# Optimization experiments

Measured on AMD Instinct MI355X. Metric: run time of the kernel, lower is better.

Reference implementation:

```python
import jax, jax.numpy as jnp
import numpy as np

LEVELS = 6
_S = float(1.0 / np.sqrt(2.0))  # forward transform scales kernels by 1/sqrt(2)
# Complex Daubechies 6-tap filters (real, imag), pre-scaled for the forward DWT.
LO_R = [v * _S for v in (-0.0662912607, 0.1104854346, 0.6629126074, 0.6629126074, 0.1104854346, -0.0662912607)]
LO_I = [v * _S for v in (-0.0855816496, -0.0855816496, 0.1711632992, 0.1711632992, -0.0855816496, -0.0855816496)]
HI_R = [v * _S for v in (-0.0662912607, -0.1104854346, 0.6629126074, -0.6629126074, 0.1104854346, 0.0662912607)]
HI_I = [v * _S for v in (0.0855816496, -0.0855816496, -0.1711632992, 0.1711632992, 0.0855816496, -0.0855816496)]


def _corr_down(v, k):
    """Circular-padded 6-tap correlation along last axis, stride-2 decimation.
    v: [..., L] (L even) -> [..., L//2]. Matches torch: circular pad 3 each side,
    valid conv (L+1 outputs), then slice 0:-1:2."""
    L = v.shape[-1]
    vp = jnp.concatenate([v[..., -3:], v, v[..., :3]], axis=-1)  # [..., L+6]
    out = k[0] * vp[..., 0:L - 1:2]
    for t in range(1, 6):
        out = out + k[t] * vp[..., t:t + L - 1:2]
    return out


def _cconv_down(xr, xi, kr, ki):
    """Complex conv + downsample: (xr + i*xi) * (kr + i*ki) along last axis."""
    return (_corr_down(xr, kr) - _corr_down(xi, ki),
            _corr_down(xr, ki) + _corr_down(xi, kr))


def _decompose(xr, xi):
    """One DWT level. xr, xi: [B, C, h, w] -> (zr, zi) same shape."""
    # vertical pass: convolve along h (transpose so h is last)
    xrT = xr.swapaxes(-1, -2)  # [B, C, w, h]
    xiT = xi.swapaxes(-1, -2)
    lr, li = _cconv_down(xrT, xiT, LO_R, LO_I)  # [B, C, w, h//2]
    hr, hi = _cconv_down(xrT, xiT, HI_R, HI_I)
    yr = jnp.concatenate([lr, hr], axis=-1).swapaxes(-1, -2)  # [B, C, h, w]
    yi = jnp.concatenate([li, hi], axis=-1).swapaxes(-1, -2)
    # horizontal pass: convolve along w
    lr, li = _cconv_down(yr, yi, LO_R, LO_I)  # [B, C, h, w//2]
    hr, hi = _cconv_down(yr, yi, HI_R, HI_I)
    zr = jnp.concatenate([lr, hr], axis=-1)
    zi = jnp.concatenate([li, hi], axis=-1)
    return zr, zi


def setup_inputs() -> dict:
    key = jax.random.key(0)
    images = jax.random.uniform(key, (8, 3, 1024, 1024), dtype=jnp.float32)
    return {"images": images}


def reference(images):
    B, C, H, W = images.shape
    xr = images
    xi = jnp.zeros_like(images)
    res_r = jnp.zeros((B, C, H, W), images.dtype)
    res_i = jnp.zeros((B, C, H, W), images.dtype)
    for i in range(LEVELS):
        h, w = H >> i, W >> i
        if i == 0:
            sr, si = xr, xi
        else:
            sr, si = res_r[..., :h, :w], res_i[..., :h, :w]
        dr, di = _decompose(sr, si)
        res_r = res_r.at[..., :h, :w].set(dr)
        res_i = res_i.at[..., :h, :w].set(di)
    return jnp.stack([res_r, res_i], axis=2)  # [B, C, 2, H, W]
```

## Files before the change

kernel.cpp:

```cpp
#include <hip/hip_runtime.h>
#include <type_traits>


#define SQ2 0.7071067811865476

constexpr float kLOR0 = (float)(-0.0662912607 * SQ2);
constexpr float kLOR1 = (float)( 0.1104854346 * SQ2);
constexpr float kLOR2 = (float)( 0.6629126074 * SQ2);
constexpr float kLOI0 = (float)(-0.0855816496 * SQ2);
constexpr float kLOI1 = (float)(-0.0855816496 * SQ2);
constexpr float kLOI2 = (float)( 0.1711632992 * SQ2);
constexpr float kHIR0 = (float)(-0.0662912607 * SQ2);
constexpr float kHIR1 = (float)(-0.1104854346 * SQ2);
constexpr float kHIR2 = (float)( 0.6629126074 * SQ2);
constexpr float kHII0 = (float)( 0.0855816496 * SQ2);
constexpr float kHII1 = (float)(-0.0855816496 * SQ2);
constexpr float kHII2 = (float)(-0.1711632992 * SQ2);

typedef float f4v __attribute__((ext_vector_type(4)));
typedef float f2v __attribute__((ext_vector_type(2)));

template <bool IM>
__device__ __forceinline__ void cconv6(const float* xr, const float* xi,
                                       float& lr, float& li, float& hr,
                                       float& hi) {
  const float s0 = xr[0] + xr[5], s1 = xr[1] + xr[4], s2 = xr[2] + xr[3];
  const float d0 = xr[0] - xr[5], d1 = xr[1] - xr[4], d2 = xr[2] - xr[3];
  lr = kLOR0 * s0 + kLOR1 * s1 + kLOR2 * s2;
  li = kLOI0 * s0 + kLOI1 * s1 + kLOI2 * s2;
  hr = kHIR0 * d0 + kHIR1 * d1 + kHIR2 * d2;
  hi = kHII0 * d0 + kHII1 * d1 + kHII2 * d2;
  if (IM) {
    const float t0 = xi[0] + xi[5], t1 = xi[1] + xi[4], t2 = xi[2] + xi[3];
    const float e0 = xi[0] - xi[5], e1 = xi[1] - xi[4], e2 = xi[2] - xi[3];
    lr -= kLOI0 * t0 + kLOI1 * t1 + kLOI2 * t2;
    li += kLOR0 * t0 + kLOR1 * t1 + kLOR2 * t2;
    hr -= kHII0 * e0 + kHII1 * e1 + kHII2 * e2;
    hi += kHIR0 * e0 + kHIR1 * e1 + kHIR2 * e2;
  }
}

__device__ __forceinline__ void gload16(const f4v* src, f4v* ldsDst) {
  __builtin_amdgcn_global_load_lds(
      (__attribute__((address_space(1))) const void*)src,
      (__attribute__((address_space(3))) void*)ldsDst, 16, 0, 0);
}

template <int TB, bool HAS_IMAG, bool LL_TO_WS>
__global__ __launch_bounds__(256) void dwt_kernel(
    const float* __restrict__ inR, const float* __restrict__ inI,
    float* __restrict__ out, float* __restrict__ llR, float* __restrict__ llI,
    int h, int w, int tilesPerRow, int tilesPerPlane, int cpx8, int HW,
    int W0) {
  constexpr int RROWS = 2 * TB + 4;
  constexpr int F4PR = TB / 2 + 2;
  constexpr int SW = 4 * F4PR;
  constexpr int NF4 = RROWS * F4PR;
  constexpr int NF4P = ((NF4 + 255) / 256) * 256;
  constexpr int C2 = 2 * TB + 4;
  constexpr int NPASS = TB / 16;
  constexpr int QACT = (TB / 2 < 16) ? TB / 2 : 16;

  __shared__ f4v s4R[NF4P];
  __shared__ f4v s4I[HAS_IMAG ? NF4P : 1];
  __shared__ __align__(16) float yLR[16 * C2], yLI[16 * C2];
  __shared__ __align__(16) float yHR[16 * C2], yHI[16 * C2];

  const int tid = threadIdx.x;
  int bid = (int)blockIdx.x;
  bid = (bid & 7) * cpx8 + (bid >> 3);
  const int plane = bid / tilesPerPlane;
  const int trem = bid - plane * tilesPerPlane;
  const int ti = trem / tilesPerRow;
  const int tj = trem - ti * tilesPerRow;

  const int hm = h - 1;
  const int w4 = w >> 2, w4m = w4 - 1;
  const int rowstart = 2 * TB * ti - 3;
  const int col4start = (TB / 2) * tj - 1;

  const float* pinR = inR + (size_t)plane * h * w;
  const float* pinI = HAS_IMAG ? (inI + (size_t)plane * h * w) : nullptr;

  {
    const int lane = tid & 63;
    const int wid = tid >> 6;
    for (int c0 = wid * 64; c0 < NF4P; c0 += 256) {
      const int idx = c0 + lane;
      const int rr = idx / F4PR;
      const int qq = idx - rr * F4PR;
      const int gr = (rowstart + rr) & hm;
      const int gq = (col4start + qq) & w4m;
      const size_t goff = (size_t)gr * w4 + gq;
      gload16((const f4v*)pinR + goff, &s4R[c0]);
      if (HAS_IMAG) gload16((const f4v*)pinI + goff, &s4I[c0]);
    }
  }
  __syncthreads();

  const float* sRf = (const float*)s4R;
  const float* sIf = (const float*)s4I;
  const int i0 = TB * ti, j0g = TB * tj;
  const int h2 = h >> 1, w2 = w >> 1;
  float* outR = out + (size_t)plane * 2 * HW;
  float* outI = outR + HW;

  const int wv = tid >> 6;
  const int lane = tid & 63;
  const int r = lane >> 4, q = lane & 15;

  for (int p = 0; p < NPASS; ++p) {
    const int ibase = p * 16 + wv * 4;

    {
      auto s2col = [&](int c) {
        const float* cR = sRf + (2 * ibase) * SW + c + 1;
        const float* cI = sIf + (2 * ibase) * SW + c + 1;
        float xr[12], xi[12];
#pragma unroll
        for (int m = 0; m < 12; ++m) {
          xr[m] = cR[m * SW];
          if (HAS_IMAG) xi[m] = cI[m * SW];
        }
#pragma unroll
        for (int k = 0; k < 4; ++k) {
          float lr, li, hr, hi;
          cconv6<HAS_IMAG>(&xr[2 * k], &xi[2 * k], lr, li, hr, hi);
          const int yi = (wv * 4 + k) * C2 + c;
          yLR[yi] = lr;
          yLI[yi] = li;
          yHR[yi] = hr;
          yHI[yi] = hi;
        }
      };
      if (C2 >= 64) {
        s2col(lane);
        if (lane < 4 * (C2 - 64)) {
          const int ce = 64 + (lane >> 2);
          const int ke = lane & 3;
          const float* cR = sRf + (2 * (ibase + ke)) * SW + ce + 1;
          const float* cI = sIf + (2 * (ibase + ke)) * SW + ce + 1;
          float xr[6], xi[6];
#pragma unroll
          for (int m = 0; m < 6; ++m) {
            xr[m] = cR[m * SW];
            if (HAS_IMAG) xi[m] = cI[m * SW];
          }
          float lr, li, hr, hi;
          cconv6<HAS_IMAG>(xr, xi, lr, li, hr, hi);
          const int yi = (wv * 4 + ke) * C2 + ce;
          yLR[yi] = lr;
          yLI[yi] = li;
          yHR[yi] = hr;
          yHI[yi] = hi;
        }
      } else {
        if (lane < C2) s2col(lane);
      }
    }
    asm volatile("s_waitcnt lgkmcnt(0)" ::: "memory");
    __builtin_amdgcn_sched_barrier(0);

    if (q < QACT) {
      const int slot = wv * 4 + r;
      const int base = slot * C2 + 4 * q;
      float xLR[8], xLI[8], xHR[8], xHI[8];
      *(f4v*)&xLR[0] = *(const f4v*)&yLR[base];
      *(f4v*)&xLR[4] = *(const f4v*)&yLR[base + 4];
      *(f4v*)&xLI[0] = *(const f4v*)&yLI[base];
      *(f4v*)&xLI[4] = *(const f4v*)&yLI[base + 4];
      *(f4v*)&xHR[0] = *(const f4v*)&yHR[base];
      *(f4v*)&xHR[4] = *(const f4v*)&yHR[base + 4];
      *(f4v*)&xHI[0] = *(const f4v*)&yHI[base];
      *(f4v*)&xHI[4] = *(const f4v*)&yHI[base + 4];
      float o[8][2];
#pragma unroll
      for (int u = 0; u < 2; ++u) {
        cconv6<true>(&xLR[2 * u], &xLI[2 * u], o[0][u], o[1][u], o[2][u],
                     o[3][u]);
        cconv6<true>(&xHR[2 * u], &xHI[2 * u], o[4][u], o[5][u], o[6][u],
                     o[7][u]);
      }
      const int gi = i0 + ibase + r;
      const int gj = j0g + 2 * q;
      const int rlo = gi, rhi = h2 + gi, clo = gj, chi = w2 + gj;
      auto st = [&](float* pdst, int v) {
        f2v t;
        t.x = o[v][0];
        t.y = o[v][1];
        __builtin_nontemporal_store(t, (f2v*)pdst);
      };
      st(outR + (size_t)rlo * W0 + chi, 2);
      st(outI + (size_t)rlo * W0 + chi, 3);
      st(outR + (size_t)rhi * W0 + clo, 4);
      st(outI + (size_t)rhi * W0 + clo, 5);
      st(outR + (size_t)rhi * W0 + chi, 6);
      st(outI + (size_t)rhi * W0 + chi, 7);
      if (LL_TO_WS) {
        const size_t off = (size_t)plane * h2 * w2 + (size_t)gi * w2 + gj;
        f2v a, b;
        a.x = o[0][0];
        a.y = o[0][1];
        b.x = o[1][0];
        b.y = o[1][1];
        *(f2v*)(llR + off) = a;
        *(f2v*)(llI + off) = b;
      } else {
        st(outR + (size_t)rlo * W0 + clo, 0);
        st(outI + (size_t)rlo * W0 + clo, 1);
      }
    }
  }
}

extern "C" void kernel_launch(void* const* d_in, const int* in_sizes, int n_in,
                              void* d_out, int out_size, void* d_ws,
                              size_t ws_size, hipStream_t stream) {
  const float* images = (const float*)d_in[0];
  float* out = (float*)d_out;
  constexpr int B = 8, C = 3, H = 1024, W = 1024;
  constexpr int NP = B * C;

  float* wsf = (float*)d_ws;
  const size_t S0 = (size_t)NP * 512 * 512;
  const size_t S1 = (size_t)NP * 256 * 256;
  float* buf0R = wsf;
  float* buf0I = wsf + S0;
  float* buf1R = wsf + 2 * S0;
  float* buf1I = wsf + 2 * S0 + S1;

  auto launch = [&](auto tb_tag, bool hasImag, bool llToWs, const float* iR,
                    const float* iI, float* lR, float* lI, int hsz) {
    constexpr int TB = decltype(tb_tag)::value;
    const int tpr = (hsz / 2) / TB;
    const int tpp = tpr * tpr;
    const int grid = NP * tpp;
    if (!hasImag) {
      dwt_kernel<TB, false, true><<<grid, 256, 0, stream>>>(
          iR, nullptr, out, lR, lI, hsz, hsz, tpr, tpp, grid / 8, H * W, W);
    } else if (llToWs) {
      dwt_kernel<TB, true, true><<<grid, 256, 0, stream>>>(
          iR, iI, out, lR, lI, hsz, hsz, tpr, tpp, grid / 8, H * W, W);
    } else {
      dwt_kernel<TB, true, false><<<grid, 256, 0, stream>>>(
          iR, iI, out, nullptr, nullptr, hsz, hsz, tpr, tpp, grid / 8, H * W,
          W);
    }
  };

  launch(std::integral_constant<int, 32>{}, false, true, images, nullptr,
         buf0R, buf0I, 1024);
  launch(std::integral_constant<int, 32>{}, true, true, buf0R, buf0I, buf1R,
         buf1I, 512);
  launch(std::integral_constant<int, 32>{}, true, true, buf1R, buf1I, buf0R,
         buf0I, 256);
  launch(std::integral_constant<int, 32>{}, true, true, buf0R, buf0I, buf1R,
         buf1I, 128);
  launch(std::integral_constant<int, 16>{}, true, true, buf1R, buf1I, buf0R,
         buf0I, 64);
  launch(std::integral_constant<int, 16>{}, true, false, buf0R, buf0I,
         nullptr, nullptr, 32);
}
```

Before: 89.02 us.

## Repartition per-wave work to two rows and one output column per lane

```diff
diff --git a/kernel.cpp b/kernel.cpp
--- a/kernel.cpp
+++ b/kernel.cpp
@@ -58,13 +58,12 @@
   constexpr int NF4 = RROWS * F4PR;
   constexpr int NF4P = ((NF4 + 255) / 256) * 256;
   constexpr int C2 = 2 * TB + 4;
-  constexpr int NPASS = TB / 16;
-  constexpr int QACT = (TB / 2 < 16) ? TB / 2 : 16;
+  constexpr int NPASS = TB / 8;
 
   __shared__ f4v s4R[NF4P];
   __shared__ f4v s4I[HAS_IMAG ? NF4P : 1];
-  __shared__ __align__(16) float yLR[16 * C2], yLI[16 * C2];
-  __shared__ __align__(16) float yHR[16 * C2], yHI[16 * C2];
+  __shared__ __align__(16) float yLR[8 * C2], yLI[8 * C2];
+  __shared__ __align__(16) float yHR[8 * C2], yHI[8 * C2];
 
   const int tid = threadIdx.x;
   int bid = (int)blockIdx.x;
@@ -107,107 +106,81 @@
 
   const int wv = tid >> 6;
   const int lane = tid & 63;
-  const int r = lane >> 4, q = lane & 15;
+  const int j = lane % TB;
+  const int rr3 = lane / TB;
 
   for (int p = 0; p < NPASS; ++p) {
-    const int ibase = p * 16 + wv * 4;
+    const int ib = p * 8 + wv * 2;
 
     {
-      auto s2col = [&](int c) {
-        const float* cR = sRf + (2 * ibase) * SW + c + 1;
-        const float* cI = sIf + (2 * ibase) * SW + c + 1;
-        float xr[12], xi[12];
+      const float* bR = sRf + (2 * ib) * SW;
+      const float* bI = sIf + (2 * ib) * SW;
+      auto docol = [&](int c) {
+        float xr[8], xi[8];
 #pragma unroll
-        for (int m = 0; m < 12; ++m) {
-          xr[m] = cR[m * SW];
-          if (HAS_IMAG) xi[m] = cI[m * SW];
+        for (int m = 0; m < 8; ++m) {
+          xr[m] = bR[m * SW + c + 1];
+          if (HAS_IMAG) xi[m] = bI[m * SW + c + 1];
         }
 #pragma unroll
-        for (int k = 0; k < 4; ++k) {
+        for (int k = 0; k < 2; ++k) {
           float lr, li, hr, hi;
           cconv6<HAS_IMAG>(&xr[2 * k], &xi[2 * k], lr, li, hr, hi);
-          const int yi = (wv * 4 + k) * C2 + c;
+          const int yi = (wv * 2 + k) * C2 + c;
           yLR[yi] = lr;
           yLI[yi] = li;
           yHR[yi] = hr;
           yHI[yi] = hi;
         }
       };
-      if (C2 >= 64) {
-        s2col(lane);
-        if (lane < 4 * (C2 - 64)) {
-          const int ce = 64 + (lane >> 2);
-          const int ke = lane & 3;
-          const float* cR = sRf + (2 * (ibase + ke)) * SW + ce + 1;
-          const float* cI = sIf + (2 * (ibase + ke)) * SW + ce + 1;
-          float xr[6], xi[6];
-#pragma unroll
-          for (int m = 0; m < 6; ++m) {
-            xr[m] = cR[m * SW];
-            if (HAS_IMAG) xi[m] = cI[m * SW];
-          }
-          float lr, li, hr, hi;
-          cconv6<HAS_IMAG>(xr, xi, lr, li, hr, hi);
-          const int yi = (wv * 4 + ke) * C2 + ce;
-          yLR[yi] = lr;
-          yLI[yi] = li;
-          yHR[yi] = hr;
-          yHI[yi] = hi;
-        }
+      if (C2 > 64) {
+        docol(lane);
+        if (lane < C2 - 64) docol(64 + lane);
       } else {
-        if (lane < C2) s2col(lane);
+        if (lane < C2) docol(lane);
       }
     }
     asm volatile("s_waitcnt lgkmcnt(0)" ::: "memory");
     __builtin_amdgcn_sched_barrier(0);
 
-    if (q < QACT) {
-      const int slot = wv * 4 + r;
-      const int base = slot * C2 + 4 * q;
-      float xLR[8], xLI[8], xHR[8], xHI[8];
-      *(f4v*)&xLR[0] = *(const f4v*)&yLR[base];
-      *(f4v*)&xLR[4] = *(const f4v*)&yLR[base + 4];
-      *(f4v*)&xLI[0] = *(const f4v*)&yLI[base];
-      *(f4v*)&xLI[4] = *(const f4v*)&yLI[base + 4];
-      *(f4v*)&xHR[0] = *(const f4v*)&yHR[base];
-      *(f4v*)&xHR[4] = *(const f4v*)&yHR[base + 4];
-      *(f4v*)&xHI[0] = *(const f4v*)&yHI[base];
-      *(f4v*)&xHI[4] = *(const f4v*)&yHI[base + 4];
-      float o[8][2];
-#pragma unroll
-      for (int u = 0; u < 2; ++u) {
-        cconv6<true>(&xLR[2 * u], &xLI[2 * u], o[0][u], o[1][u], o[2][u],
-                     o[3][u]);
-        cconv6<true>(&xHR[2 * u], &xHI[2 * u], o[4][u], o[5][u], o[6][u],
-                     o[7][u]);
-      }
-      const int gi = i0 + ibase + r;
-      const int gj = j0g + 2 * q;
+    if (rr3 < 2) {
+      const int slot = wv * 2 + rr3;
+      const int cb = slot * C2 + 2 * j;
+      float xLR[6], xLI[6], xHR[6], xHI[6];
+      *(f2v*)&xLR[0] = *(const f2v*)&yLR[cb];
+      *(f2v*)&xLR[2] = *(const f2v*)&yLR[cb + 2];
+      *(f2v*)&xLR[4] = *(const f2v*)&yLR[cb + 4];
+      *(f2v*)&xLI[0] = *(const f2v*)&yLI[cb];
+      *(f2v*)&xLI[2] = *(const f2v*)&yLI[cb + 2];
+      *(f2v*)&xLI[4] = *(const f2v*)&yLI[cb + 4];
+      *(f2v*)&xHR[0] = *(const f2v*)&yHR[cb];
+      *(f2v*)&xHR[2] = *(const f2v*)&yHR[cb + 2];
+      *(f2v*)&xHR[4] = *(const f2v*)&yHR[cb + 4];
+      *(f2v*)&xHI[0] = *(const f2v*)&yHI[cb];
+      *(f2v*)&xHI[2] = *(const f2v*)&yHI[cb + 2];
+      *(f2v*)&xHI[4] = *(const f2v*)&yHI[cb + 4];
+      float llr, lli, lhr, lhi, hlr, hli, hhr, hhi;
+      cconv6<true>(xLR, xLI, llr, lli, lhr, lhi);
+      cconv6<true>(xHR, xHI, hlr, hli, hhr, hhi);
+      const int gi = i0 + ib + rr3;
+      const int gj = j0g + j;
       const int rlo = gi, rhi = h2 + gi, clo = gj, chi = w2 + gj;
-      auto st = [&](float* pdst, int v) {
-        f2v t;
-        t.x = o[v][0];
-        t.y = o[v][1];
-        __builtin_nontemporal_store(t, (f2v*)pdst);
+      auto st1 = [&](float* pdst, float v) {
+        __builtin_nontemporal_store(v, pdst);
       };
-      st(outR + (size_t)rlo * W0 + chi, 2);
-      st(outI + (size_t)rlo * W0 + chi, 3);
-      st(outR + (size_t)rhi * W0 + clo, 4);
-      st(outI + (size_t)rhi * W0 + clo, 5);
-      st(outR + (size_t)rhi * W0 + chi, 6);
-      st(outI + (size_t)rhi * W0 + chi, 7);
+      st1(outR + (size_t)rlo * W0 + chi, lhr);
+      st1(outI + (size_t)rlo * W0 + chi, lhi);
+      st1(outR + (size_t)rhi * W0 + clo, hlr);
+      st1(outI + (size_t)rhi * W0 + clo, hli);
+      st1(outR + (size_t)rhi * W0 + chi, hhr);
+      st1(outI + (size_t)rhi * W0 + chi, hhi);
       if (LL_TO_WS) {
         const size_t off = (size_t)plane * h2 * w2 + (size_t)gi * w2 + gj;
-        f2v a, b;
-        a.x = o[0][0];
-        a.y = o[0][1];
-        b.x = o[1][0];
-        b.y = o[1][1];
-        *(f2v*)(llR + off) = a;
-        *(f2v*)(llI + off) = b;
+        llR[off] = llr;
+        llI[off] = lli;
       } else {
-        st(outR + (size_t)rlo * W0 + clo, 0);
-        st(outI + (size_t)rlo * W0 + clo, 1);
+        st1(outR + (size_t)rlo * W0 + clo, llr);
+        st1(outI + (size_t)rlo * W0 + clo, lli);
       }
     }
   }
```

Measured after the change: 91.98 us. 3.3% more time.
